# Kernel optimization log

Hardware: AMD Instinct MI355X
Metric: run time of the kernel (lower is better)

## Reference

```python
import jax, jax.numpy as jnp
import numpy as np

SIZE, D, N, E = 50000, 1024, 50000, 100000


def setup_inputs() -> dict:
    key = jax.random.key(0)
    k1, k2 = jax.random.split(key)
    # torchhd.embeddings.Random produces bipolar {-1,+1} MAP hypervectors
    w = jnp.where(jax.random.uniform(k1, (SIZE, D)) < 0.5, -1.0, 1.0).astype(jnp.float32)
    edge_index = jax.random.randint(k2, (2, E), 0, N, dtype=jnp.int32)
    return {"node_ids_weight": w, "edge_index": edge_index, "num_nodes": N}


def reference(node_ids_weight, edge_index, num_nodes):
    # degree_centrality: in-degree via bincount on columns, normalized
    col = edge_index[1]
    degree = jnp.bincount(col, length=num_nodes)
    pr = degree / num_nodes  # float
    pr_argsort = jnp.argsort(pr)  # stable sort, matches torch sort semantics on ties

    # node_id_hvs[pr_argsort] = weight[:num_nodes]  (scatter assign)
    node_id_hvs = jnp.zeros((num_nodes, node_ids_weight.shape[1]),
                            dtype=node_ids_weight.dtype)
    node_id_hvs = node_id_hvs.at[pr_argsort].set(node_ids_weight[:num_nodes])

    # to_undirected: sort endpoints per edge, then unique columns.
    # jit-friendly unique: lexsort edges, mask out duplicates of the previous edge.
    e = jnp.sort(edge_index, axis=0)  # [2, E], row <= col per edge
    order = jnp.lexsort((e[1], e[0]))
    r = e[0][order]
    c = e[1][order]
    keep = jnp.concatenate([
        jnp.array([True]),
        (r[1:] != r[:-1]) | (c[1:] != c[:-1]),
    ])  # [E] True for first occurrence of each unique edge

    # bind = elementwise multiply of gathered hvs; multiset = sum over edges
    hvs = node_id_hvs[r] * node_id_hvs[c]  # [E, D]
    out = jnp.sum(jnp.where(keep[:, None], hvs, 0.0), axis=0)  # [D]
    return out
```

## Files before the change

kernel.cpp:

```cpp
#include <hip/hip_runtime.h>
#include <stdint.h>

#define DCAP   128
#define CHUNK  1024
#define LOG_TAB 19
#define TAB_SIZE (1u << LOG_TAB)
#define TAB_MASK (TAB_SIZE - 1u)
#define KEMPTY 0xFFFFFFFFu

__global__ void k_degree(const int* __restrict__ col, int* __restrict__ degree, int E) {
    int e = blockIdx.x * blockDim.x + threadIdx.x;
    if (e < E) atomicAdd(&degree[col[e]], 1);
}

__global__ void k_chunk_hist(const int* __restrict__ degree, int* __restrict__ hist,
                             int* __restrict__ chunkHist, int N) {
    __shared__ int sh[DCAP];
    int t = threadIdx.x;
    if (t < DCAP) sh[t] = 0;
    __syncthreads();
    int j = blockIdx.x * CHUNK + t;
    if (j < N) {
        int d = degree[j];
        if (d < DCAP) atomicAdd(&sh[d], 1);
        else          atomicAdd(&hist[d], 1);
    }
    __syncthreads();
    if (t < DCAP) chunkHist[blockIdx.x * DCAP + t] = sh[t];
}

__global__ void k_chunk_prefix(int* __restrict__ hist, int* __restrict__ chunkHist,
                               int numChunks) {
    __shared__ int stot[DCAP];
    int d = threadIdx.x;
    int tot = 0;
    for (int c = 0; c < numChunks; ++c) tot += chunkHist[c * DCAP + d];
    stot[d] = tot;
    hist[d] = tot;
    __syncthreads();
    int run = 0;
    for (int d2 = 0; d2 < d; ++d2) run += stot[d2];
    for (int c = 0; c < numChunks; ++c) {
        int tmp = chunkHist[c * DCAP + d];
        chunkHist[c * DCAP + d] = run;
        run += tmp;
    }
}

__global__ __launch_bounds__(CHUNK) void k_pos(const int* __restrict__ degree,
                                               const int* __restrict__ chunkBase,
                                               const int* __restrict__ hist,
                                               int* __restrict__ pos,
                                               int N, int E, int numChunks) {
    int t = threadIdx.x;
    if ((int)blockIdx.x < numChunks) {
        __shared__ int sdeg[CHUNK];
        int j = blockIdx.x * CHUNK + t;
        int d = (j < N) ? degree[j] : -1;
        sdeg[t] = d;
        __syncthreads();
        if (j < N && d < DCAP && d >= 0) {
            int r = 0;
            for (int t2 = 0; t2 < t; ++t2) r += (sdeg[t2] == d);
            pos[j] = chunkBase[blockIdx.x * DCAP + d] + r;
        }
    } else {
        int d = DCAP + (blockIdx.x - numChunks) * CHUNK + t;
        if (d > E) return;
        if (hist[d] == 0) return;
        int base = 0;
        for (int d2 = 0; d2 < d; ++d2) base += hist[d2];
        int cnt = 0;
        for (int j = 0; j < N; ++j)
            if (degree[j] == d) pos[j] = base + cnt++;
    }
}

#define PACK_DEPTH 8
__global__ __launch_bounds__(256) void k_pack_ballot(const float* __restrict__ W,
                                                     uint32_t* __restrict__ Wbits,
                                                     long long G) {
    long long wv0 = ((long long)blockIdx.x * 256 + threadIdx.x) >> 6;
    long long nwv = ((long long)gridDim.x * 256) >> 6;
    int lane = threadIdx.x & 63;
    int k = lane >> 1, half = lane & 1;
    const uint4* W4 = (const uint4*)W;
    for (long long gb = wv0 * PACK_DEPTH; gb < G; gb += nwv * PACK_DEPTH) {
        uint4 u[PACK_DEPTH];
        #pragma unroll
        for (int s = 0; s < PACK_DEPTH; ++s) {
            long long g = gb + s;
            if (g >= G) g = G - 1;
            u[s] = W4[g * 64 + lane];
        }
        #pragma unroll
        for (int s = 0; s < PACK_DEPTH; ++s) {
            long long g = gb + s;
            unsigned long long m0 = __ballot((int)u[s].x < 0);
            unsigned long long m1 = __ballot((int)u[s].y < 0);
            unsigned long long m2 = __ballot((int)u[s].z < 0);
            unsigned long long m3 = __ballot((int)u[s].w < 0);
            if (g < G && lane < 8) {
                unsigned long long m = (k == 0) ? m0 : (k == 1) ? m1
                                     : (k == 2) ? m2 : m3;
                Wbits[g * 8 + lane] = half ? (uint32_t)(m >> 32) : (uint32_t)m;
            }
        }
    }
}

__global__ __launch_bounds__(256) void k_pack_linear(const float* __restrict__ W,
                                                     uint32_t* __restrict__ Wbits, long long NW) {
    long long widx = (long long)blockIdx.x * 256 + threadIdx.x;
    if (widx >= NW) return;
    const uint4* src = (const uint4*)(W + widx * 32);
    uint32_t word = 0;
    #pragma unroll
    for (int q = 0; q < 8; ++q) {
        uint4 u = src[q];
        word |= (u.x >> 31) << (4 * q + 0);
        word |= (u.y >> 31) << (4 * q + 1);
        word |= (u.z >> 31) << (4 * q + 2);
        word |= (u.w >> 31) << (4 * q + 3);
    }
    Wbits[widx] = word;
}

__global__ void k_insert(const int* __restrict__ ei, const int* __restrict__ pos,
                         unsigned int* __restrict__ tab, int* __restrict__ uA,
                         int* __restrict__ uB, int* __restrict__ count, int E) {
    int e = blockIdx.x * blockDim.x + threadIdx.x;
    if (e >= E) return;
    int a = ei[e], b = ei[E + e];
    int r = min(a, b), c = max(a, b);
    unsigned int key = ((unsigned int)r << 16) | (unsigned int)c;
    unsigned int h = (key * 2654435761u) >> (32 - LOG_TAB);
    while (true) {
        unsigned int old = atomicCAS(&tab[h], KEMPTY, key);
        if (old == KEMPTY) {
            int idx = atomicAdd(count, 1);
            uA[idx] = pos[r];
            uB[idx] = pos[c];
            return;
        }
        if (old == key) return;
        h = (h + 1) & TAB_MASK;
    }
}

__global__ __launch_bounds__(256) void k_accum_bits(const uint32_t* __restrict__ Wbits,
                                                    const int* __restrict__ uA,
                                                    const int* __restrict__ uB,
                                                    const int* __restrict__ count,
                                                    int* __restrict__ neg, int D) {
    __shared__ int sneg[1024];
    int t = threadIdx.x;
    int w = t & 31;
    int slot = t >> 5;
    int wpr = D / 32;
    for (int i = t; i < D; i += 256) sneg[i] = 0;
    __syncthreads();
    int cnt = *count;
    int cnts[32];
    #pragma unroll
    for (int d = 0; d < 32; ++d) cnts[d] = 0;
    for (int base = blockIdx.x * 8; base < cnt; base += gridDim.x * 8) {
        int e = base + slot;
        if (e < cnt) {
            uint32_t a = Wbits[(size_t)uA[e] * wpr + w];
            uint32_t b = Wbits[(size_t)uB[e] * wpr + w];
            uint32_t x = a ^ b;
            #pragma unroll
            for (int d = 0; d < 32; ++d) cnts[d] += (x >> d) & 1u;
        }
    }
    #pragma unroll
    for (int d = 0; d < 32; ++d) atomicAdd(&sneg[w * 32 + d], cnts[d]);
    __syncthreads();
    for (int i = t; i < D; i += 256)
        if (sneg[i]) atomicAdd(&neg[i], sneg[i]);
}

__global__ void k_finalize(const int* __restrict__ neg, const int* __restrict__ count,
                           float* __restrict__ out, int D, int permuted) {
    int d = blockIdx.x * blockDim.x + threadIdx.x;
    if (d >= D) return;
    int ni;
    if (permuted) {
        int off = d & 255, q = d >> 8;
        int k = off & 3, l = off >> 2, half = l >> 5, b = l & 31;
        ni = (q * 8 + 2 * k + half) * 32 + b;
    } else {
        ni = d;
    }
    out[d] = (float)(*count - 2 * neg[ni]);
}

static inline size_t align256(size_t x) { return (x + 255) & ~(size_t)255; }

extern "C" void kernel_launch(void* const* d_in, const int* in_sizes, int n_in,
                              void* d_out, int out_size, void* d_ws, size_t ws_size,
                              hipStream_t stream) {
    const float* W  = (const float*)d_in[0];
    const int*   ei = (const int*)d_in[1];
    const int D = out_size;
    const int N = in_sizes[0] / D;
    const int E = in_sizes[1] / 2;
    const int numChunks = (N + CHUNK - 1) / CHUNK;
    const long long ND = (long long)N * D;
    const long long NW = ND / 32;

    char* p = (char*)d_ws;
    char* zbase = p;
    int* degree       = (int*)p;          p += align256((size_t)N * 4);
    int* hist         = (int*)p;          p += align256((size_t)(E + 1) * 4);
    int* count        = (int*)p;          p += 256;
    int* neg          = (int*)p;          p += align256((size_t)D * 4);
    size_t zbytes = (size_t)(p - zbase);
    int* chunkHist    = (int*)p;          p += align256((size_t)numChunks * DCAP * 4);
    int* pos          = (int*)p;          p += align256((size_t)N * 4);
    unsigned int* tab = (unsigned int*)p; p += (size_t)TAB_SIZE * 4;
    int* uA           = (int*)p;          p += align256((size_t)E * 4);
    int* uB           = (int*)p;          p += align256((size_t)E * 4);
    uint32_t* Wbits   = (uint32_t*)p;     p += align256((size_t)NW * 4);

    hipMemsetAsync(zbase, 0, zbytes, stream);
    hipMemsetAsync(tab, 0xFF, (size_t)TAB_SIZE * 4, stream);

    k_degree<<<(E + 255) / 256, 256, 0, stream>>>(ei + E, degree, E);
    k_chunk_hist<<<numChunks, CHUNK, 0, stream>>>(degree, hist, chunkHist, N);
    k_chunk_prefix<<<1, DCAP, 0, stream>>>(hist, chunkHist, numChunks);
    int nLargeBlocks = (E + 1 - DCAP + CHUNK - 1) / CHUNK;
    k_pos<<<numChunks + nLargeBlocks, CHUNK, 0, stream>>>(degree, chunkHist, hist,
                                                          pos, N, E, numChunks);

    int permuted = (D % 256 == 0);
    if (permuted) {
        long long G = ND / 256;
        k_pack_ballot<<<2048, 256, 0, stream>>>(W, Wbits, G);
    } else {
        k_pack_linear<<<(int)((NW + 255) / 256), 256, 0, stream>>>(W, Wbits, NW);
    }

    k_insert<<<(E + 255) / 256, 256, 0, stream>>>(ei, pos, tab, uA, uB, count, E);
    k_accum_bits<<<1024, 256, 0, stream>>>(Wbits, uA, uB, count, neg, D);
    k_finalize<<<(D + 255) / 256, 256, 0, stream>>>(neg, count, (float*)d_out, D, permuted);
}
```

Measured before the change: 137.2 us.

## Fuse preprocessing stages into persistent cooperative kernel with grid barriers and interleaved packing

Replaces the chain of memsets and small preprocessing kernels (degree count, chunk histogram, prefix, position, hash insert, bit packing) with one persistent cooperative kernel. The stages are separated by a sharded global barrier, and slices of the bit-packing work are interleaved between them so packing bandwidth overlaps the latency-bound phases. The hash insert now stores raw node ids, and the accumulation kernel looks up positions indirectly. This removes many launch gaps, but adds barrier spin overhead, atomic-based loads, and reliance on all blocks being co-resident.

Result: slower. 257.2 us (median of 2 runs) (+87.4%).

```diff
diff --git a/kernel.cpp b/kernel.cpp
--- a/kernel.cpp
+++ b/kernel.cpp
@@ -7,12 +7,225 @@
 #define TAB_SIZE (1u << LOG_TAB)
 #define TAB_MASK (TAB_SIZE - 1u)
 #define KEMPTY 0xFFFFFFFFu
+#define NSHARD 64
+
+typedef unsigned int uintv4 __attribute__((ext_vector_type(4)));
+
+__device__ __forceinline__ void gbar(int* bar, int* gen, int NB, int phase) {
+    __syncthreads();
+    if (threadIdx.x == 0)
+        atomicAdd(&bar[(blockIdx.x & (NSHARD - 1)) << 5], 1);
+    if (blockIdx.x == 0) {
+        if (threadIdx.x < 64) {
+            int target = NB * phase;
+            for (;;) {
+                int s = atomicAdd(&bar[threadIdx.x << 5], 0);
+                #pragma unroll
+                for (int off = 32; off > 0; off >>= 1) s += __shfl_down(s, off);
+                s = __shfl(s, 0);
+                if (s >= target) break;
+                __builtin_amdgcn_s_sleep(8);
+            }
+            atomicExch(&gen[threadIdx.x << 5], phase);
+        }
+    } else if (threadIdx.x == 0) {
+        int* mg = &gen[(blockIdx.x & (NSHARD - 1)) << 5];
+        while (atomicAdd(mg, 0) < phase) __builtin_amdgcn_s_sleep(64);
+    }
+    __syncthreads();
+}
+
+__device__ __forceinline__ void packSlice(const float* __restrict__ W,
+                                          uint32_t* __restrict__ Wbits,
+                                          long long lo, long long hi,
+                                          int NB, int firstBlock) {
+    if ((int)blockIdx.x < firstBlock) return;
+    long long wv  = (((long long)((int)blockIdx.x - firstBlock)) * 256 + threadIdx.x) >> 6;
+    long long nwv = (((long long)(NB - firstBlock)) * 256) >> 6;
+    int lane = threadIdx.x & 63;
+    int k = lane >> 1, half = lane & 1;
+    const uintv4* W4 = (const uintv4*)W;
+    for (long long g = lo + wv; g < hi; g += nwv) {
+        uintv4 u = W4[g * 64 + lane];
+        unsigned long long m0 = __ballot((int)u.x < 0);
+        unsigned long long m1 = __ballot((int)u.y < 0);
+        unsigned long long m2 = __ballot((int)u.z < 0);
+        unsigned long long m3 = __ballot((int)u.w < 0);
+        if (lane < 8) {
+            unsigned long long m = (k == 0) ? m0 : (k == 1) ? m1 : (k == 2) ? m2 : m3;
+            Wbits[g * 8 + lane] = half ? (uint32_t)(m >> 32) : (uint32_t)m;
+        }
+    }
+}
+
+__global__ __launch_bounds__(256, 8) void k_mega(
+    const float* __restrict__ W, const int* __restrict__ ei,
+    int* degree, int* hist, int* chunkHist, int* pos,
+    unsigned int* tab, int* uA, int* uB, int* count,
+    int* neg, uint32_t* Wbits, int* bar, int* gen,
+    int N, int E, int D, int numChunks, int nLargeBlocks, long long G, int NB)
+{
+    __shared__ int smem[CHUNK];
+    const int tid = threadIdx.x;
+    const long long TT = (long long)NB * 256;
+    const long long gt = (long long)blockIdx.x * 256 + tid;
+
+    for (long long j = gt; j < N; j += TT) atomicExch(&degree[j], 0);
+    for (long long j = gt; j < E + 1; j += TT) atomicExch(&hist[j], 0);
+    if (gt == 0) atomicExch(count, 0);
+    for (long long j = gt; j < D; j += TT) neg[j] = 0;
+    for (long long j = gt; j < (long long)TAB_SIZE; j += TT) atomicExch(&tab[j], KEMPTY);
+    packSlice(W, Wbits, 0, G / 5, NB, 0);
+    gbar(bar, gen, NB, 1);
+
+    for (long long e = gt; e < E; e += TT) {
+        int a = ei[e], b = ei[E + e];
+        atomicAdd(&degree[b], 1);
+        int r = min(a, b), c = max(a, b);
+        unsigned int key = ((unsigned int)r << 16) | (unsigned int)c;
+        unsigned int h = (key * 2654435761u) >> (32 - LOG_TAB);
+        for (;;) {
+            unsigned int old = atomicCAS(&tab[h], KEMPTY, key);
+            if (old == KEMPTY) { int idx = atomicAdd(count, 1); uA[idx] = r; uB[idx] = c; break; }
+            if (old == key) break;
+            h = (h + 1) & TAB_MASK;
+        }
+    }
+    packSlice(W, Wbits, G / 5, 2 * G / 5, NB, 0);
+    gbar(bar, gen, NB, 2);
+
+    if ((int)blockIdx.x < numChunks) {
+        if (tid < DCAP) smem[tid] = 0;
+        __syncthreads();
+        for (int q = 0; q < CHUNK / 256; ++q) {
+            int j = blockIdx.x * CHUNK + q * 256 + tid;
+            if (j < N) {
+                int d = atomicAdd(&degree[j], 0);
+                if (d < DCAP) atomicAdd(&smem[d], 1);
+                else          atomicAdd(&hist[d], 1);
+            }
+        }
+        __syncthreads();
+        if (tid < DCAP) atomicExch(&chunkHist[blockIdx.x * DCAP + tid], smem[tid]);
+    }
+    packSlice(W, Wbits, 2 * G / 5, 3 * G / 5, NB, 0);
+    gbar(bar, gen, NB, 3);
+
+    if (blockIdx.x == 0) {
+        int tot = 0;
+        if (tid < DCAP) {
+            for (int c0 = 0; c0 < numChunks; c0 += 8) {
+                int v[8];
+                #pragma unroll
+                for (int i = 0; i < 8; ++i)
+                    v[i] = (c0 + i < numChunks) ? atomicAdd(&chunkHist[(c0 + i) * DCAP + tid], 0) : 0;
+                #pragma unroll
+                for (int i = 0; i < 8; ++i) tot += v[i];
+            }
+            smem[tid] = tot;
+            atomicExch(&hist[tid], tot);
+        }
+        __syncthreads();
+        if (tid < DCAP) {
+            int run = 0;
+            for (int d2 = 0; d2 < tid; ++d2) run += smem[d2];
+            for (int c0 = 0; c0 < numChunks; c0 += 8) {
+                int v[8];
+                #pragma unroll
+                for (int i = 0; i < 8; ++i)
+                    v[i] = (c0 + i < numChunks) ? atomicAdd(&chunkHist[(c0 + i) * DCAP + tid], 0) : 0;
+                #pragma unroll
+                for (int i = 0; i < 8; ++i)
+                    if (c0 + i < numChunks) { atomicExch(&chunkHist[(c0 + i) * DCAP + tid], run); run += v[i]; }
+            }
+        }
+    }
+    packSlice(W, Wbits, 3 * G / 5, 4 * G / 5, NB, 1);
+    gbar(bar, gen, NB, 4);
+
+    if ((int)blockIdx.x < numChunks) {
+        for (int q = 0; q < CHUNK / 256; ++q) {
+            int j = blockIdx.x * CHUNK + q * 256 + tid;
+            smem[q * 256 + tid] = (j < N) ? atomicAdd(&degree[j], 0) : -1;
+        }
+        __syncthreads();
+        int base0 = blockIdx.x * CHUNK;
+        for (int q = 0; q < CHUNK / 256; ++q) {
+            int idx = tid * (CHUNK / 256) + q;
+            int j = base0 + idx;
+            int d = smem[idx];
+            if (j < N && d >= 0 && d < DCAP) {
+                int r = 0;
+                for (int t2 = 0; t2 < idx; ++t2) r += (smem[t2] == d);
+                pos[j] = atomicAdd(&chunkHist[blockIdx.x * DCAP + d], 0) + r;
+            }
+        }
+    } else if ((int)blockIdx.x < numChunks + nLargeBlocks) {
+        int d = DCAP + ((int)blockIdx.x - numChunks) * 256 + tid;
+        if (d <= E && atomicAdd(&hist[d], 0) != 0) {
+            int base = 0;
+            for (int d2 = 0; d2 < d; ++d2) base += atomicAdd(&hist[d2], 0);
+            int cnt2 = 0;
+            for (int j = 0; j < N; ++j)
+                if (atomicAdd(&degree[j], 0) == d) { pos[j] = base + cnt2; ++cnt2; }
+        }
+    }
+    packSlice(W, Wbits, 4 * G / 5, G, NB, numChunks + nLargeBlocks);
+}
+
+__global__ __launch_bounds__(256) void k_accum_bits(const uint32_t* __restrict__ Wbits,
+                                                    const int* __restrict__ pos,
+                                                    const int* __restrict__ uA,
+                                                    const int* __restrict__ uB,
+                                                    const int* __restrict__ count,
+                                                    int* __restrict__ neg, int D) {
+    __shared__ int sneg[1024];
+    int t = threadIdx.x, w = t & 31, slot = t >> 5;
+    int wpr = D / 32;
+    for (int i = t; i < D; i += 256) sneg[i] = 0;
+    __syncthreads();
+    int cnt = *count;
+    int cnts[32];
+    #pragma unroll
+    for (int d = 0; d < 32; ++d) cnts[d] = 0;
+    if (w < wpr) {
+        for (int base = blockIdx.x * 8; base < cnt; base += gridDim.x * 8) {
+            int e = base + slot;
+            if (e < cnt) {
+                size_t ra = (size_t)pos[uA[e]] * wpr;
+                size_t rb = (size_t)pos[uB[e]] * wpr;
+                uint32_t x = Wbits[ra + w] ^ Wbits[rb + w];
+                #pragma unroll
+                for (int d = 0; d < 32; ++d) cnts[d] += (x >> d) & 1u;
+            }
+        }
+        #pragma unroll
+        for (int d = 0; d < 32; ++d) atomicAdd(&sneg[w * 32 + d], cnts[d]);
+    }
+    __syncthreads();
+    for (int i = t; i < D; i += 256)
+        if (sneg[i]) atomicAdd(&neg[i], sneg[i]);
+}
+
+__global__ void k_finalize(const int* __restrict__ neg, const int* __restrict__ count,
+                           float* __restrict__ out, int D, int permuted) {
+    int d = blockIdx.x * blockDim.x + threadIdx.x;
+    if (d >= D) return;
+    int ni;
+    if (permuted) {
+        int off = d & 255, q = d >> 8;
+        int k = off & 3, l = off >> 2, half = l >> 5, b = l & 31;
+        ni = (q * 8 + 2 * k + half) * 32 + b;
+    } else {
+        ni = d;
+    }
+    out[d] = (float)(*count - 2 * neg[ni]);
+}
 
 __global__ void k_degree(const int* __restrict__ col, int* __restrict__ degree, int E) {
     int e = blockIdx.x * blockDim.x + threadIdx.x;
     if (e < E) atomicAdd(&degree[col[e]], 1);
 }
-
 __global__ void k_chunk_hist(const int* __restrict__ degree, int* __restrict__ hist,
                              int* __restrict__ chunkHist, int N) {
     __shared__ int sh[DCAP];
@@ -28,7 +241,6 @@
     __syncthreads();
     if (t < DCAP) chunkHist[blockIdx.x * DCAP + t] = sh[t];
 }
-
 __global__ void k_chunk_prefix(int* __restrict__ hist, int* __restrict__ chunkHist,
                                int numChunks) {
     __shared__ int stot[DCAP];
@@ -46,7 +258,6 @@
         run += tmp;
     }
 }
-
 __global__ __launch_bounds__(CHUNK) void k_pos(const int* __restrict__ degree,
                                                const int* __restrict__ chunkBase,
                                                const int* __restrict__ hist,
@@ -75,49 +286,35 @@
             if (degree[j] == d) pos[j] = base + cnt++;
     }
 }
-
-#define PACK_DEPTH 8
 __global__ __launch_bounds__(256) void k_pack_ballot(const float* __restrict__ W,
                                                      uint32_t* __restrict__ Wbits,
                                                      long long G) {
-    long long wv0 = ((long long)blockIdx.x * 256 + threadIdx.x) >> 6;
+    long long wv = ((long long)blockIdx.x * 256 + threadIdx.x) >> 6;
     long long nwv = ((long long)gridDim.x * 256) >> 6;
     int lane = threadIdx.x & 63;
     int k = lane >> 1, half = lane & 1;
-    const uint4* W4 = (const uint4*)W;
-    for (long long gb = wv0 * PACK_DEPTH; gb < G; gb += nwv * PACK_DEPTH) {
-        uint4 u[PACK_DEPTH];
-        #pragma unroll
-        for (int s = 0; s < PACK_DEPTH; ++s) {
-            long long g = gb + s;
-            if (g >= G) g = G - 1;
-            u[s] = W4[g * 64 + lane];
-        }
-        #pragma unroll
-        for (int s = 0; s < PACK_DEPTH; ++s) {
-            long long g = gb + s;
-            unsigned long long m0 = __ballot((int)u[s].x < 0);
-            unsigned long long m1 = __ballot((int)u[s].y < 0);
-            unsigned long long m2 = __ballot((int)u[s].z < 0);
-            unsigned long long m3 = __ballot((int)u[s].w < 0);
-            if (g < G && lane < 8) {
-                unsigned long long m = (k == 0) ? m0 : (k == 1) ? m1
-                                     : (k == 2) ? m2 : m3;
-                Wbits[g * 8 + lane] = half ? (uint32_t)(m >> 32) : (uint32_t)m;
-            }
-        }
-    }
-}
-
+    const uintv4* W4 = (const uintv4*)W;
+    for (long long g = wv; g < G; g += nwv) {
+        uintv4 u = W4[g * 64 + lane];
+        unsigned long long m0 = __ballot((int)u.x < 0);
+        unsigned long long m1 = __ballot((int)u.y < 0);
+        unsigned long long m2 = __ballot((int)u.z < 0);
+        unsigned long long m3 = __ballot((int)u.w < 0);
+        if (lane < 8) {
+            unsigned long long m = (k == 0) ? m0 : (k == 1) ? m1 : (k == 2) ? m2 : m3;
+            Wbits[g * 8 + lane] = half ? (uint32_t)(m >> 32) : (uint32_t)m;
+        }
+    }
+}
 __global__ __launch_bounds__(256) void k_pack_linear(const float* __restrict__ W,
                                                      uint32_t* __restrict__ Wbits, long long NW) {
     long long widx = (long long)blockIdx.x * 256 + threadIdx.x;
     if (widx >= NW) return;
-    const uint4* src = (const uint4*)(W + widx * 32);
+    const uintv4* src = (const uintv4*)(W + widx * 32);
     uint32_t word = 0;
     #pragma unroll
     for (int q = 0; q < 8; ++q) {
-        uint4 u = src[q];
+        uintv4 u = src[q];
         word |= (u.x >> 31) << (4 * q + 0);
         word |= (u.y >> 31) << (4 * q + 1);
         word |= (u.z >> 31) << (4 * q + 2);
@@ -125,10 +322,9 @@
     }
     Wbits[widx] = word;
 }
-
-__global__ void k_insert(const int* __restrict__ ei, const int* __restrict__ pos,
-                         unsigned int* __restrict__ tab, int* __restrict__ uA,
-                         int* __restrict__ uB, int* __restrict__ count, int E) {
+__global__ void k_insert_nodes(const int* __restrict__ ei, unsigned int* __restrict__ tab,
+                               int* __restrict__ uA, int* __restrict__ uB,
+                               int* __restrict__ count, int E) {
     int e = blockIdx.x * blockDim.x + threadIdx.x;
     if (e >= E) return;
     int a = ei[e], b = ei[E + e];
@@ -137,63 +333,10 @@
     unsigned int h = (key * 2654435761u) >> (32 - LOG_TAB);
     while (true) {
         unsigned int old = atomicCAS(&tab[h], KEMPTY, key);
-        if (old == KEMPTY) {
-            int idx = atomicAdd(count, 1);
-            uA[idx] = pos[r];
-            uB[idx] = pos[c];
-            return;
-        }
+        if (old == KEMPTY) { int idx = atomicAdd(count, 1); uA[idx] = r; uB[idx] = c; return; }
         if (old == key) return;
         h = (h + 1) & TAB_MASK;
     }
-}
-
-__global__ __launch_bounds__(256) void k_accum_bits(const uint32_t* __restrict__ Wbits,
-                                                    const int* __restrict__ uA,
-                                                    const int* __restrict__ uB,
-                                                    const int* __restrict__ count,
-                                                    int* __restrict__ neg, int D) {
-    __shared__ int sneg[1024];
-    int t = threadIdx.x;
-    int w = t & 31;
-    int slot = t >> 5;
-    int wpr = D / 32;
-    for (int i = t; i < D; i += 256) sneg[i] = 0;
-    __syncthreads();
-    int cnt = *count;
-    int cnts[32];
-    #pragma unroll
-    for (int d = 0; d < 32; ++d) cnts[d] = 0;
-    for (int base = blockIdx.x * 8; base < cnt; base += gridDim.x * 8) {
-        int e = base + slot;
-        if (e < cnt) {
-            uint32_t a = Wbits[(size_t)uA[e] * wpr + w];
-            uint32_t b = Wbits[(size_t)uB[e] * wpr + w];
-            uint32_t x = a ^ b;
-            #pragma unroll
-            for (int d = 0; d < 32; ++d) cnts[d] += (x >> d) & 1u;
-        }
-    }
-    #pragma unroll
-    for (int d = 0; d < 32; ++d) atomicAdd(&sneg[w * 32 + d], cnts[d]);
-    __syncthreads();
-    for (int i = t; i < D; i += 256)
-        if (sneg[i]) atomicAdd(&neg[i], sneg[i]);
-}
-
-__global__ void k_finalize(const int* __restrict__ neg, const int* __restrict__ count,
-                           float* __restrict__ out, int D, int permuted) {
-    int d = blockIdx.x * blockDim.x + threadIdx.x;
-    if (d >= D) return;
-    int ni;
-    if (permuted) {
-        int off = d & 255, q = d >> 8;
-        int k = off & 3, l = off >> 2, half = l >> 5, b = l & 31;
-        ni = (q * 8 + 2 * k + half) * 32 + b;
-    } else {
-        ni = d;
-    }
-    out[d] = (float)(*count - 2 * neg[ni]);
 }
 
 static inline size_t align256(size_t x) { return (x + 255) & ~(size_t)255; }
@@ -207,10 +350,14 @@
     const int N = in_sizes[0] / D;
     const int E = in_sizes[1] / 2;
     const int numChunks = (N + CHUNK - 1) / CHUNK;
+    const int nLargeBlocks256 = (E + 1 - DCAP + 255) / 256;
     const long long ND = (long long)N * D;
     const long long NW = ND / 32;
+    const long long G  = ND / 256;
 
     char* p = (char*)d_ws;
+    int* bar          = (int*)p;          p += NSHARD * 32 * 4;
+    int* gen          = (int*)p;          p += NSHARD * 32 * 4;
     char* zbase = p;
     int* degree       = (int*)p;          p += align256((size_t)N * 4);
     int* hist         = (int*)p;          p += align256((size_t)(E + 1) * 4);
@@ -224,25 +371,52 @@
     int* uB           = (int*)p;          p += align256((size_t)E * 4);
     uint32_t* Wbits   = (uint32_t*)p;     p += align256((size_t)NW * 4);
 
-    hipMemsetAsync(zbase, 0, zbytes, stream);
-    hipMemsetAsync(tab, 0xFF, (size_t)TAB_SIZE * 4, stream);
-
-    k_degree<<<(E + 255) / 256, 256, 0, stream>>>(ei + E, degree, E);
-    k_chunk_hist<<<numChunks, CHUNK, 0, stream>>>(degree, hist, chunkHist, N);
-    k_chunk_prefix<<<1, DCAP, 0, stream>>>(hist, chunkHist, numChunks);
-    int nLargeBlocks = (E + 1 - DCAP + CHUNK - 1) / CHUNK;
-    k_pos<<<numChunks + nLargeBlocks, CHUNK, 0, stream>>>(degree, chunkHist, hist,
-                                                          pos, N, E, numChunks);
-
-    int permuted = (D % 256 == 0);
-    if (permuted) {
-        long long G = ND / 256;
-        k_pack_ballot<<<2048, 256, 0, stream>>>(W, Wbits, G);
+    int dev = 0;
+    hipGetDevice(&dev);
+    int cus = 0;
+    hipDeviceGetAttribute(&cus, hipDeviceAttributeMultiprocessorCount, dev);
+    int maxB = 0;
+    hipOccupancyMaxActiveBlocksPerMultiprocessor(&maxB, k_mega, 256, 0);
+    int NB = cus * maxB;
+    if (NB > 2048) NB = 2048;
+
+    bool useMega = (D % 256 == 0) && (D <= 1024) &&
+                   (NB >= numChunks + nLargeBlocks256 + 64);
+
+    if (useMega) {
+        hipMemsetAsync(bar, 0, NSHARD * 32 * 4 * 2, stream);
+        const float* Wp = W; const int* eip = ei;
+        int Np = N, Ep = E, Dp = D, nc = numChunks, nl = nLargeBlocks256, nb = NB;
+        long long Gp = G;
+        void* args[] = { (void*)&Wp, (void*)&eip, (void*)&degree, (void*)&hist,
+                         (void*)&chunkHist, (void*)&pos, (void*)&tab, (void*)&uA,
+                         (void*)&uB, (void*)&count, (void*)&neg, (void*)&Wbits,
+                         (void*)&bar, (void*)&gen, (void*)&Np, (void*)&Ep,
+                         (void*)&Dp, (void*)&nc, (void*)&nl, (void*)&Gp, (void*)&nb };
+        hipError_t err = hipLaunchCooperativeKernel((void*)k_mega, dim3(NB), dim3(256),
+                                                    args, 0, stream);
+        if (err != hipSuccess) {
+            (void)hipGetLastError();
+            k_mega<<<NB, 256, 0, stream>>>(W, ei, degree, hist, chunkHist, pos, tab,
+                                           uA, uB, count, neg, Wbits, bar, gen,
+                                           N, E, D, numChunks, nLargeBlocks256, G, NB);
+        }
+        k_accum_bits<<<2048, 256, 0, stream>>>(Wbits, pos, uA, uB, count, neg, D);
+        k_finalize<<<(D + 255) / 256, 256, 0, stream>>>(neg, count, (float*)d_out, D, 1);
     } else {
-        k_pack_linear<<<(int)((NW + 255) / 256), 256, 0, stream>>>(W, Wbits, NW);
-    }
-
-    k_insert<<<(E + 255) / 256, 256, 0, stream>>>(ei, pos, tab, uA, uB, count, E);
-    k_accum_bits<<<1024, 256, 0, stream>>>(Wbits, uA, uB, count, neg, D);
-    k_finalize<<<(D + 255) / 256, 256, 0, stream>>>(neg, count, (float*)d_out, D, permuted);
-}
+        hipMemsetAsync(zbase, 0, zbytes, stream);
+        hipMemsetAsync(tab, 0xFF, (size_t)TAB_SIZE * 4, stream);
+        k_degree<<<(E + 255) / 256, 256, 0, stream>>>(ei + E, degree, E);
+        k_chunk_hist<<<numChunks, CHUNK, 0, stream>>>(degree, hist, chunkHist, N);
+        k_chunk_prefix<<<1, DCAP, 0, stream>>>(hist, chunkHist, numChunks);
+        int nLB = (E + 1 - DCAP + CHUNK - 1) / CHUNK;
+        k_pos<<<numChunks + nLB, CHUNK, 0, stream>>>(degree, chunkHist, hist, pos,
+                                                     N, E, numChunks);
+        int permuted = (D % 256 == 0);
+        if (permuted) k_pack_ballot<<<2048, 256, 0, stream>>>(W, Wbits, G);
+        else          k_pack_linear<<<(int)((NW + 255) / 256), 256, 0, stream>>>(W, Wbits, NW);
+        k_insert_nodes<<<(E + 255) / 256, 256, 0, stream>>>(ei, tab, uA, uB, count, E);
+        k_accum_bits<<<2048, 256, 0, stream>>>(Wbits, pos, uA, uB, count, neg, D);
+        k_finalize<<<(D + 255) / 256, 256, 0, stream>>>(neg, count, (float*)d_out, D, permuted);
+    }
+}
```

## Fuse degree count with edge dedup insert and fold chunk prefix into pos kernel

Applied to the files above, without the earlier changes.

Merges the degree-count kernel and the hash-table edge insertion into one pass over edge_index, storing raw node ids and resolving pos[] indirection later inside the accumulation kernel. The single-block chunk-prefix kernel is removed: each k_pos chunk block now recomputes per-degree totals and its own prefix from chunkHist, and large-degree bases are computed as suffix sums. The accumulate grid is doubled. This cuts two launches and one serial kernel, at the cost of redundant prefix work per block and an extra dependent gather in the hot loop.

Result: slower. 145.0 us (+5.7%).

```diff
diff --git a/kernel.cpp b/kernel.cpp
--- a/kernel.cpp
+++ b/kernel.cpp
@@ -8,13 +8,33 @@
 #define TAB_MASK (TAB_SIZE - 1u)
 #define KEMPTY 0xFFFFFFFFu
 
-__global__ void k_degree(const int* __restrict__ col, int* __restrict__ degree, int E) {
+typedef unsigned int uintv4 __attribute__((ext_vector_type(4)));
+
+__global__ void k_deg_ins(const int* __restrict__ ei, int* __restrict__ degree,
+                          unsigned int* __restrict__ tab, int* __restrict__ uA,
+                          int* __restrict__ uB, int* __restrict__ count, int E) {
     int e = blockIdx.x * blockDim.x + threadIdx.x;
-    if (e < E) atomicAdd(&degree[col[e]], 1);
-}
-
-__global__ void k_chunk_hist(const int* __restrict__ degree, int* __restrict__ hist,
-                             int* __restrict__ chunkHist, int N) {
+    if (e >= E) return;
+    int a = ei[e], b = ei[E + e];
+    atomicAdd(&degree[b], 1);
+    int r = min(a, b), c = max(a, b);
+    unsigned int key = ((unsigned int)r << 16) | (unsigned int)c;
+    unsigned int h = (key * 2654435761u) >> (32 - LOG_TAB);
+    for (;;) {
+        unsigned int old = atomicCAS(&tab[h], KEMPTY, key);
+        if (old == KEMPTY) {
+            int idx = atomicAdd(count, 1);
+            uA[idx] = r; uB[idx] = c;
+            return;
+        }
+        if (old == key) return;
+        h = (h + 1) & TAB_MASK;
+    }
+}
+
+__global__ __launch_bounds__(CHUNK) void k_chunk_hist(const int* __restrict__ degree,
+                                                      int* __restrict__ hist,
+                                                      int* __restrict__ chunkHist, int N) {
     __shared__ int sh[DCAP];
     int t = threadIdx.x;
     if (t < DCAP) sh[t] = 0;
@@ -29,47 +49,49 @@
     if (t < DCAP) chunkHist[blockIdx.x * DCAP + t] = sh[t];
 }
 
-__global__ void k_chunk_prefix(int* __restrict__ hist, int* __restrict__ chunkHist,
-                               int numChunks) {
-    __shared__ int stot[DCAP];
-    int d = threadIdx.x;
-    int tot = 0;
-    for (int c = 0; c < numChunks; ++c) tot += chunkHist[c * DCAP + d];
-    stot[d] = tot;
-    hist[d] = tot;
-    __syncthreads();
-    int run = 0;
-    for (int d2 = 0; d2 < d; ++d2) run += stot[d2];
-    for (int c = 0; c < numChunks; ++c) {
-        int tmp = chunkHist[c * DCAP + d];
-        chunkHist[c * DCAP + d] = run;
-        run += tmp;
-    }
-}
-
 __global__ __launch_bounds__(CHUNK) void k_pos(const int* __restrict__ degree,
-                                               const int* __restrict__ chunkBase,
+                                               const int* __restrict__ chunkHist,
                                                const int* __restrict__ hist,
                                                int* __restrict__ pos,
                                                int N, int E, int numChunks) {
     int t = threadIdx.x;
     if ((int)blockIdx.x < numChunks) {
         __shared__ int sdeg[CHUNK];
-        int j = blockIdx.x * CHUNK + t;
+        __shared__ int stot[DCAP];
+        __shared__ int sbase[DCAP];
+        int me = blockIdx.x;
+        if (t < DCAP) {
+            int tot = 0, pre = 0;
+            for (int c = 0; c < numChunks; ++c) {
+                int v = chunkHist[c * DCAP + t];
+                pre += (c < me) ? v : 0;
+                tot += v;
+            }
+            stot[t] = tot;
+            sbase[t] = pre;
+        }
+        __syncthreads();
+        if (t < DCAP) {
+            int run = 0;
+            for (int d2 = 0; d2 < t; ++d2) run += stot[d2];
+            sbase[t] += run;
+        }
+        int j = me * CHUNK + t;
         int d = (j < N) ? degree[j] : -1;
         sdeg[t] = d;
         __syncthreads();
-        if (j < N && d < DCAP && d >= 0) {
+        if (j < N && d >= 0 && d < DCAP) {
             int r = 0;
             for (int t2 = 0; t2 < t; ++t2) r += (sdeg[t2] == d);
-            pos[j] = chunkBase[blockIdx.x * DCAP + d] + r;
+            pos[j] = sbase[d] + r;
         }
     } else {
-        int d = DCAP + (blockIdx.x - numChunks) * CHUNK + t;
+        int d = DCAP + ((int)blockIdx.x - numChunks) * CHUNK + t;
         if (d > E) return;
         if (hist[d] == 0) return;
-        int base = 0;
-        for (int d2 = 0; d2 < d; ++d2) base += hist[d2];
+        long long suf = 0;
+        for (int d2 = d; d2 <= E; ++d2) suf += hist[d2];
+        int base = N - (int)suf;
         int cnt = 0;
         for (int j = 0; j < N; ++j)
             if (degree[j] == d) pos[j] = base + cnt++;
@@ -84,9 +106,9 @@
     long long nwv = ((long long)gridDim.x * 256) >> 6;
     int lane = threadIdx.x & 63;
     int k = lane >> 1, half = lane & 1;
-    const uint4* W4 = (const uint4*)W;
+    const uintv4* W4 = (const uintv4*)W;
     for (long long gb = wv0 * PACK_DEPTH; gb < G; gb += nwv * PACK_DEPTH) {
-        uint4 u[PACK_DEPTH];
+        uintv4 u[PACK_DEPTH];
         #pragma unroll
         for (int s = 0; s < PACK_DEPTH; ++s) {
             long long g = gb + s;
@@ -113,11 +135,11 @@
                                                      uint32_t* __restrict__ Wbits, long long NW) {
     long long widx = (long long)blockIdx.x * 256 + threadIdx.x;
     if (widx >= NW) return;
-    const uint4* src = (const uint4*)(W + widx * 32);
+    const uintv4* src = (const uintv4*)(W + widx * 32);
     uint32_t word = 0;
     #pragma unroll
     for (int q = 0; q < 8; ++q) {
-        uint4 u = src[q];
+        uintv4 u = src[q];
         word |= (u.x >> 31) << (4 * q + 0);
         word |= (u.y >> 31) << (4 * q + 1);
         word |= (u.z >> 31) << (4 * q + 2);
@@ -126,37 +148,14 @@
     Wbits[widx] = word;
 }
 
-__global__ void k_insert(const int* __restrict__ ei, const int* __restrict__ pos,
-                         unsigned int* __restrict__ tab, int* __restrict__ uA,
-                         int* __restrict__ uB, int* __restrict__ count, int E) {
-    int e = blockIdx.x * blockDim.x + threadIdx.x;
-    if (e >= E) return;
-    int a = ei[e], b = ei[E + e];
-    int r = min(a, b), c = max(a, b);
-    unsigned int key = ((unsigned int)r << 16) | (unsigned int)c;
-    unsigned int h = (key * 2654435761u) >> (32 - LOG_TAB);
-    while (true) {
-        unsigned int old = atomicCAS(&tab[h], KEMPTY, key);
-        if (old == KEMPTY) {
-            int idx = atomicAdd(count, 1);
-            uA[idx] = pos[r];
-            uB[idx] = pos[c];
-            return;
-        }
-        if (old == key) return;
-        h = (h + 1) & TAB_MASK;
-    }
-}
-
 __global__ __launch_bounds__(256) void k_accum_bits(const uint32_t* __restrict__ Wbits,
+                                                    const int* __restrict__ pos,
                                                     const int* __restrict__ uA,
                                                     const int* __restrict__ uB,
                                                     const int* __restrict__ count,
                                                     int* __restrict__ neg, int D) {
     __shared__ int sneg[1024];
-    int t = threadIdx.x;
-    int w = t & 31;
-    int slot = t >> 5;
+    int t = threadIdx.x, w = t & 31, slot = t >> 5;
     int wpr = D / 32;
     for (int i = t; i < D; i += 256) sneg[i] = 0;
     __syncthreads();
@@ -164,18 +163,20 @@
     int cnts[32];
     #pragma unroll
     for (int d = 0; d < 32; ++d) cnts[d] = 0;
-    for (int base = blockIdx.x * 8; base < cnt; base += gridDim.x * 8) {
-        int e = base + slot;
-        if (e < cnt) {
-            uint32_t a = Wbits[(size_t)uA[e] * wpr + w];
-            uint32_t b = Wbits[(size_t)uB[e] * wpr + w];
-            uint32_t x = a ^ b;
-            #pragma unroll
-            for (int d = 0; d < 32; ++d) cnts[d] += (x >> d) & 1u;
-        }
-    }
-    #pragma unroll
-    for (int d = 0; d < 32; ++d) atomicAdd(&sneg[w * 32 + d], cnts[d]);
+    if (w < wpr) {
+        for (int base = blockIdx.x * 8; base < cnt; base += gridDim.x * 8) {
+            int e = base + slot;
+            if (e < cnt) {
+                size_t ra = (size_t)pos[uA[e]] * wpr;
+                size_t rb = (size_t)pos[uB[e]] * wpr;
+                uint32_t x = Wbits[ra + w] ^ Wbits[rb + w];
+                #pragma unroll
+                for (int d = 0; d < 32; ++d) cnts[d] += (x >> d) & 1u;
+            }
+        }
+        #pragma unroll
+        for (int d = 0; d < 32; ++d) atomicAdd(&sneg[w * 32 + d], cnts[d]);
+    }
     __syncthreads();
     for (int i = t; i < D; i += 256)
         if (sneg[i]) atomicAdd(&neg[i], sneg[i]);
@@ -209,6 +210,7 @@
     const int numChunks = (N + CHUNK - 1) / CHUNK;
     const long long ND = (long long)N * D;
     const long long NW = ND / 32;
+    const long long G  = ND / 256;
 
     char* p = (char*)d_ws;
     char* zbase = p;
@@ -227,22 +229,19 @@
     hipMemsetAsync(zbase, 0, zbytes, stream);
     hipMemsetAsync(tab, 0xFF, (size_t)TAB_SIZE * 4, stream);
 
-    k_degree<<<(E + 255) / 256, 256, 0, stream>>>(ei + E, degree, E);
+    k_deg_ins<<<(E + 255) / 256, 256, 0, stream>>>(ei, degree, tab, uA, uB, count, E);
     k_chunk_hist<<<numChunks, CHUNK, 0, stream>>>(degree, hist, chunkHist, N);
-    k_chunk_prefix<<<1, DCAP, 0, stream>>>(hist, chunkHist, numChunks);
     int nLargeBlocks = (E + 1 - DCAP + CHUNK - 1) / CHUNK;
     k_pos<<<numChunks + nLargeBlocks, CHUNK, 0, stream>>>(degree, chunkHist, hist,
                                                           pos, N, E, numChunks);
 
     int permuted = (D % 256 == 0);
     if (permuted) {
-        long long G = ND / 256;
         k_pack_ballot<<<2048, 256, 0, stream>>>(W, Wbits, G);
     } else {
         k_pack_linear<<<(int)((NW + 255) / 256), 256, 0, stream>>>(W, Wbits, NW);
     }
 
-    k_insert<<<(E + 255) / 256, 256, 0, stream>>>(ei, pos, tab, uA, uB, count, E);
-    k_accum_bits<<<1024, 256, 0, stream>>>(Wbits, uA, uB, count, neg, D);
+    k_accum_bits<<<2048, 256, 0, stream>>>(Wbits, pos, uA, uB, count, neg, D);
     k_finalize<<<(D + 255) / 256, 256, 0, stream>>>(neg, count, (float*)d_out, D, permuted);
 }
```
